# Kernel tuning notes

Hardware: AMD Instinct MI355X
Metric: run time of the kernel (lower is better)

## Reference

```python
import jax, jax.numpy as jnp
import numpy as np

N, E, D_IN, D_POS, LATENT, C = 50000, 800000, 500, 2, 128, 10
NEG_SLOPE = 0.2

def _glorot(key, shape):
    lim = np.sqrt(6.0 / (shape[0] + shape[1]))
    return jax.random.uniform(key, shape, jnp.float32, -lim, lim)

def setup_inputs() -> dict:
    key = jax.random.key(0)
    ks = jax.random.split(key, 20)
    x = jax.random.normal(ks[0], (N, D_IN), jnp.float32)
    pos = jax.random.uniform(ks[1], (N, D_POS), jnp.float32)
    edge_index = jax.random.randint(ks[2], (2, E), 0, N, jnp.int32)
    edge_attr = jax.random.uniform(ks[3], (E, 1), jnp.float32)
    d0 = D_IN + D_POS
    params = dict(
        W1=_glorot(ks[4], (d0, 512)), b1=jnp.zeros((512,)),
        W2=_glorot(ks[5], (512, 256)), b2=jnp.zeros((256,)),
        W3=_glorot(ks[6], (256, LATENT)), b3=jnp.zeros((LATENT,)),
        Wl=_glorot(ks[7], (LATENT, LATENT)), bl=jnp.zeros((LATENT,)),
        Wr=_glorot(ks[8], (LATENT, LATENT)), br=jnp.zeros((LATENT,)),
        We=_glorot(ks[9], (1, LATENT)),
        att=_glorot(ks[10], (LATENT, 1))[:, 0],
        bg=jnp.zeros((LATENT,)),
        Wd1=_glorot(ks[11], (LATENT, 64)), bd1=jnp.zeros((64,)),
        Wd2=_glorot(ks[12], (64, C)), bd2=jnp.zeros((C,)),
    )
    return dict(x=x, pos=pos, edge_index=edge_index, edge_attr=edge_attr, **params)

def _gatv2(h, src, dst, edge_attr, Wl, bl, Wr, br, We, att, bg):
    n = h.shape[0]
    xl = h @ Wl + bl            # [N, D] source transform
    xr = h @ Wr + br            # [N, D] target transform
    e = edge_attr @ We          # [E, D] edge embedding
    m = xl[src] + xr[dst] + e   # [E, D]
    m = jnp.where(m > 0, m, NEG_SLOPE * m)   # leaky_relu
    s = m @ att                 # [E] attention logits
    smax = jax.lax.stop_gradient(jax.ops.segment_max(s, dst, num_segments=n))
    ex = jnp.exp(s - smax[dst])
    denom = jax.ops.segment_sum(ex, dst, num_segments=n)
    alpha = ex / denom[dst]     # edge softmax over incoming edges
    out = jax.ops.segment_sum(alpha[:, None] * xl[src], dst, num_segments=n)
    return out + bg

def reference(x, pos, edge_index, edge_attr,
              W1, b1, W2, b2, W3, b3,
              Wl, bl, Wr, br, We, att, bg,
              Wd1, bd1, Wd2, bd2):
    xin = jnp.concatenate([x, pos], axis=-1)
    # encoder MLP [-1,512,256,latent], plain_last=True
    h = jax.nn.relu(xin @ W1 + b1)
    h = jax.nn.relu(h @ W2 + b2)
    h = h @ W3 + b3
    # GATv2 spatial channel, then block activation (plain_last=False)
    src, dst = edge_index[0], edge_index[1]
    h = _gatv2(h, src, dst, edge_attr, Wl, bl, Wr, br, We, att, bg)
    z = jax.nn.relu(h)
    # decoder MLP latent->64->C, plain_last, then softmax
    d = jax.nn.relu(z @ Wd1 + bd1)
    logits = d @ Wd2 + bd2
    return jax.nn.softmax(logits, axis=-1)
```

## Files before the change

### kernel.cpp

```cpp
#include <hip/hip_runtime.h>
#include <hip/hip_bf16.h>

#define NEG_SLOPE 0.2f

typedef _Float16 half8   __attribute__((ext_vector_type(8)));
typedef _Float16 half2v  __attribute__((ext_vector_type(2)));
typedef float    float4v __attribute__((ext_vector_type(4)));

__device__ __forceinline__ void gload16(const _Float16* g, _Float16* l)
{
    __builtin_amdgcn_global_load_lds(
        (const __attribute__((address_space(1))) unsigned int*)g,
        (__attribute__((address_space(3))) unsigned int*)l, 16, 0, 0);
}

__global__ __launch_bounds__(256)
void concat_f16_kernel(const float* __restrict__ x, const float* __restrict__ pos,
                       _Float16* __restrict__ A0, int N)
{
    const int total = N * 256;
    for (int i = blockIdx.x * 256 + threadIdx.x; i < total; i += gridDim.x * 256) {
        int node = i >> 8;
        int c2   = (i & 255) * 2;
        float2 v = make_float2(0.f, 0.f);
        if (c2 < 500)       v = *(const float2*)(x + (size_t)node * 500 + c2);
        else if (c2 == 500) v = *(const float2*)(pos + (size_t)node * 2);
        half2v h; h.x = (_Float16)v.x; h.y = (_Float16)v.y;
        *(half2v*)(A0 + (size_t)node * 512 + c2) = h;
    }
}

__global__ void wconv_kernel(const float* __restrict__ W, _Float16* __restrict__ Wt,
                             int K, int Nout, int Kpad)
{
    int total = Nout * Kpad;
    for (int i = blockIdx.x * blockDim.x + threadIdx.x; i < total;
         i += gridDim.x * blockDim.x) {
        int n = i / Kpad, k = i - n * Kpad;
        Wt[i] = (_Float16)((k < K) ? W[(size_t)k * Nout + n] : 0.f);
    }
}

__global__ __launch_bounds__(256)
void wfold_kernel(const float* __restrict__ W3, const float* __restrict__ Wl,
                  const float* __restrict__ Wr, _Float16* __restrict__ Wct)
{
    __shared__ float colv[128];
    const int nn = blockIdx.x;
    const float* Ws = (nn < 128) ? Wl : Wr;
    const int c = nn & 127;
    if (threadIdx.x < 128) colv[threadIdx.x] = Ws[threadIdx.x * 128 + c];
    __syncthreads();
    const int k2 = threadIdx.x;
    const float* wrow = W3 + k2 * 128;
    float s = 0.f;
    #pragma unroll 8
    for (int j = 0; j < 128; ++j) s += wrow[j] * colv[j];
    Wct[nn * 256 + k2] = (_Float16)s;
}

__global__ void bfold_kernel(const float* __restrict__ Wl, const float* __restrict__ Wr,
                             const float* __restrict__ b3, const float* __restrict__ bl,
                             const float* __restrict__ br, float* __restrict__ bcombo)
{
    int nn = threadIdx.x;
    const float* Ws = (nn < 128) ? Wl : Wr;
    int c = nn & 127;
    float s = (nn < 128) ? bl[c] : br[c];
    for (int j = 0; j < 128; ++j) s += b3[j] * Ws[j * 128 + c];
    bcombo[nn] = s;
}

__device__ inline void decode_swz(int b, int nblk, int ny, int& bx, int& by)
{
    int q = nblk >> 3, r = nblk & 7;
    int xcd = b & 7, j = b >> 3;
    int L = (xcd < r ? xcd * (q + 1) : r * (q + 1) + (xcd - r) * q) + j;
    bx = L / ny;
    by = L - bx * ny;
}

template<int WF32, int WF16>
__global__ __launch_bounds__(256)
void gemm_f16_kernel(const _Float16* __restrict__ A, const _Float16* __restrict__ Bt,
                     const float* __restrict__ bias, float* __restrict__ Cf,
                     _Float16* __restrict__ Ch, int M, int N, int K, int ny, int do_relu)
{
    __shared__ __align__(16) _Float16 smem[3][8192];

    int bx, by;
    decode_swz(blockIdx.x, gridDim.x, ny, bx, by);

    const int t    = threadIdx.x;
    const int row0 = bx * 128;
    const int n0   = by * 128;
    const int lane = t & 63;
    const int w    = t >> 6;
    const int wrow = (w >> 1) * 64;
    const int wcol = (w & 1) * 64;
    const int lrow = lane & 15;
    const int lk   = lane >> 4;
    const int sw   = lk ^ ((lrow >> 1) & 3);

    const int rl     = lane >> 2;
    const int lk_log = (lane & 3) ^ ((lane >> 3) & 3);

    int rA0 = row0 + w * 16 + rl;        if (rA0 > M - 1) rA0 = M - 1;
    int rA1 = row0 + (w + 4) * 16 + rl;  if (rA1 > M - 1) rA1 = M - 1;
    int rB0 = n0 + w * 16 + rl;          if (rB0 > N - 1) rB0 = N - 1;
    int rB1 = n0 + (w + 4) * 16 + rl;    if (rB1 > N - 1) rB1 = N - 1;

    const _Float16* gA0 = A  + (size_t)rA0 * K + lk_log * 8;
    const _Float16* gA1 = A  + (size_t)rA1 * K + lk_log * 8;
    const _Float16* gB0 = Bt + (size_t)rB0 * K + lk_log * 8;
    const _Float16* gB1 = Bt + (size_t)rB1 * K + lk_log * 8;

    float4v acc[4][4];
    #pragma unroll
    for (int i = 0; i < 4; ++i)
        #pragma unroll
        for (int j = 0; j < 4; ++j)
            acc[i][j] = (float4v){0.f, 0.f, 0.f, 0.f};

    const int KT = K >> 5;

    auto stage = [&](int kt, int buf) {
        _Float16* sA = &smem[buf][0];
        _Float16* sB = &smem[buf][4096];
        int ko = kt * 32;
        gload16(gA0 + ko, sA + (w    ) * 512);
        gload16(gA1 + ko, sA + (w + 4) * 512);
        gload16(gB0 + ko, sB + (w    ) * 512);
        gload16(gB1 + ko, sB + (w + 4) * 512);
    };

    stage(0, 0);
    if (KT > 1) {
        stage(1, 1);
        asm volatile("s_waitcnt vmcnt(4)" ::: "memory");
    } else {
        asm volatile("s_waitcnt vmcnt(0)" ::: "memory");
    }
    __builtin_amdgcn_sched_barrier(0);
    __builtin_amdgcn_s_barrier();

    for (int kt = 0; kt < KT; ++kt) {
        if (kt + 2 < KT) stage(kt + 2, (kt + 2) % 3);

        const _Float16* bufA = &smem[kt % 3][0];
        const _Float16* bufB = &smem[kt % 3][4096];

        half8 af[4], bf[4];
        #pragma unroll
        for (int mi = 0; mi < 4; ++mi)
            af[mi] = *(const half8*)(bufA + (wrow + mi * 16 + lrow) * 32 + sw * 8);
        #pragma unroll
        for (int ni = 0; ni < 4; ++ni)
            bf[ni] = *(const half8*)(bufB + (wcol + ni * 16 + lrow) * 32 + sw * 8);

        #pragma unroll
        for (int mi = 0; mi < 4; ++mi)
            #pragma unroll
            for (int ni = 0; ni < 4; ++ni)
                acc[mi][ni] = __builtin_amdgcn_mfma_f32_16x16x32_f16(
                    af[mi], bf[ni], acc[mi][ni], 0, 0, 0);

        if (kt + 1 < KT) {
            if (kt + 2 < KT) asm volatile("s_waitcnt vmcnt(4)" ::: "memory");
            else             asm volatile("s_waitcnt vmcnt(0)" ::: "memory");
            __builtin_amdgcn_sched_barrier(0);
            __builtin_amdgcn_s_barrier();
        }
    }

    #pragma unroll
    for (int mi = 0; mi < 4; ++mi) {
        #pragma unroll
        for (int ni = 0; ni < 4; ++ni) {
            #pragma unroll
            for (int r = 0; r < 4; ++r) {
                int row = row0 + wrow + mi * 16 + lk * 4 + r;
                int col = n0 + wcol + ni * 16 + lrow;
                if (row < M && col < N) {
                    float v = acc[mi][ni][r] + bias[col];
                    if (do_relu) v = fmaxf(v, 0.f);
                    if (WF32) Cf[(size_t)row * N + col] = v;
                    if (WF16) Ch[(size_t)row * N + col] = (_Float16)v;
                }
            }
        }
    }
}

__global__ __launch_bounds__(256)
void dec_fused_kernel(const _Float16* __restrict__ zh, const _Float16* __restrict__ Wd1t,
                      const float* __restrict__ bd1, const float* __restrict__ Wd2,
                      const float* __restrict__ bd2, float* __restrict__ out, int n)
{
    __shared__ __align__(16) _Float16 zs[128 * 40];
    __shared__ __align__(16) _Float16 wd1s[64 * 136];
    __shared__ __align__(16) _Float16 dsd[128 * 66];
    __shared__ float wd2s[640];
    __shared__ float bd1s[64];
    __shared__ float bd2s[10];

    const int t    = threadIdx.x;
    const int lane = t & 63;
    const int w    = t >> 6;
    const int wrow = (w >> 1) * 64;
    const int wcol = (w & 1) * 32;
    const int lrow = lane & 15;
    const int lk   = lane >> 4;
    const int node0 = blockIdx.x * 128;

    for (int i = t; i < 64 * 16; i += 256) {
        int r = i >> 4, c8 = i & 15;
        *(half8*)&wd1s[r * 136 + c8 * 8] = *(const half8*)(Wd1t + r * 128 + c8 * 8);
    }
    for (int i = t; i < 640; i += 256) wd2s[i] = Wd2[i];
    if (t < 64) bd1s[t] = bd1[t];
    if (t < 10) bd2s[t] = bd2[t];

    float4v acc[4][2];
    #pragma unroll
    for (int i = 0; i < 4; ++i)
        #pragma unroll
        for (int j = 0; j < 2; ++j)
            acc[i][j] = (float4v){0.f, 0.f, 0.f, 0.f};

    const int zrow = t >> 1;
    const int ch   = t & 1;
    int gz = node0 + zrow; if (gz > n - 1) gz = n - 1;
    const _Float16* zsrc = zh + (size_t)gz * 128 + ch * 16;

    for (int kt = 0; kt < 4; ++kt) {
        __syncthreads();
        *(half8*)&zs[zrow * 40 + ch * 16]     = *(const half8*)(zsrc + kt * 32);
        *(half8*)&zs[zrow * 40 + ch * 16 + 8] = *(const half8*)(zsrc + kt * 32 + 8);
        __syncthreads();

        half8 af[4], bf[2];
        #pragma unroll
        for (int mi = 0; mi < 4; ++mi)
            af[mi] = *(const half8*)&zs[(wrow + mi * 16 + lrow) * 40 + lk * 8];
        #pragma unroll
        for (int ni = 0; ni < 2; ++ni)
            bf[ni] = *(const half8*)&wd1s[(wcol + ni * 16 + lrow) * 136 + kt * 32 + lk * 8];

        #pragma unroll
        for (int mi = 0; mi < 4; ++mi)
            #pragma unroll
            for (int ni = 0; ni < 2; ++ni)
                acc[mi][ni] = __builtin_amdgcn_mfma_f32_16x16x32_f16(
                    af[mi], bf[ni], acc[mi][ni], 0, 0, 0);
    }

    #pragma unroll
    for (int mi = 0; mi < 4; ++mi) {
        #pragma unroll
        for (int ni = 0; ni < 2; ++ni) {
            #pragma unroll
            for (int r = 0; r < 4; ++r) {
                int rr = wrow + mi * 16 + lk * 4 + r;
                int cc = wcol + ni * 16 + lrow;
                float v = fmaxf(acc[mi][ni][r] + bd1s[cc], 0.f);
                dsd[rr * 66 + cc] = (_Float16)v;
            }
        }
    }
    __syncthreads();

    if (t < 128) {
        int node = node0 + t;
        if (node < n) {
            float lg[10];
            #pragma unroll
            for (int c = 0; c < 10; ++c) lg[c] = bd2s[c];
            #pragma unroll
            for (int k8 = 0; k8 < 8; ++k8) {
                half8 dv = *(const half8*)&dsd[t * 66 + k8 * 8];
                #pragma unroll
                for (int j = 0; j < 8; ++j) {
                    float dj = (float)dv[j];
                    #pragma unroll
                    for (int c = 0; c < 10; ++c)
                        lg[c] += dj * wd2s[(k8 * 8 + j) * 10 + c];
                }
            }
            float mx = lg[0];
            #pragma unroll
            for (int c = 1; c < 10; ++c) mx = fmaxf(mx, lg[c]);
            float ssum = 0.f;
            #pragma unroll
            for (int c = 0; c < 10; ++c) { lg[c] = expf(lg[c] - mx); ssum += lg[c]; }
            float inv = 1.f / ssum;
            #pragma unroll
            for (int c = 0; c < 10; ++c)
                out[(size_t)node * 10 + c] = lg[c] * inv;
        }
    }
}

__global__ void init_cnt_kernel(int* cnt, int n)
{
    for (int i = blockIdx.x * blockDim.x + threadIdx.x; i < n;
         i += gridDim.x * blockDim.x)
        cnt[i] = 0;
}

__global__ void count_edges_kernel(const int* __restrict__ dst, int* cnt, int E)
{
    int e = blockIdx.x * blockDim.x + threadIdx.x;
    if (e < E) atomicAdd(&cnt[dst[e]], 1);
}

__global__ __launch_bounds__(256)
void block_sum_kernel(const int* __restrict__ cnt, int* __restrict__ bsum, int n)
{
    __shared__ int sh[256];
    int t = threadIdx.x;
    int i = blockIdx.x * 256 + t;
    sh[t] = (i < n) ? cnt[i] : 0;
    __syncthreads();
    #pragma unroll
    for (int off = 128; off > 0; off >>= 1) {
        if (t < off) sh[t] += sh[t + off];
        __syncthreads();
    }
    if (t == 0) bsum[blockIdx.x] = sh[0];
}

__global__ __launch_bounds__(256)
void scan_bsum_kernel(int* __restrict__ bsum, int* __restrict__ row_start, int nb, int n)
{
    __shared__ int sh[256];
    int t = threadIdx.x;
    int v = (t < nb) ? bsum[t] : 0;
    sh[t] = v;
    __syncthreads();
    #pragma unroll
    for (int off = 1; off < 256; off <<= 1) {
        int xv = (t >= off) ? sh[t - off] : 0;
        __syncthreads();
        sh[t] += xv;
        __syncthreads();
    }
    if (t < nb) bsum[t] = sh[t] - v;
    if (t == 255) row_start[n] = sh[255];
}

__global__ __launch_bounds__(256)
void scan_final_kernel(const int* __restrict__ cnt, const int* __restrict__ boff,
                       int* __restrict__ row_start, int* __restrict__ cursor, int n)
{
    __shared__ int sh[256];
    int t = threadIdx.x;
    int i = blockIdx.x * 256 + t;
    int v = (i < n) ? cnt[i] : 0;
    sh[t] = v;
    __syncthreads();
    #pragma unroll
    for (int off = 1; off < 256; off <<= 1) {
        int xv = (t >= off) ? sh[t - off] : 0;
        __syncthreads();
        sh[t] += xv;
        __syncthreads();
    }
    if (i < n) {
        int ex = boff[blockIdx.x] + sh[t] - v;
        row_start[i] = ex;
        cursor[i]    = ex;
    }
}

__global__ void scatter_edges_kernel(const int* __restrict__ dst, const int* __restrict__ src,
                                     const float* __restrict__ ea, int* cursor,
                                     int2* __restrict__ recs, int E)
{
    int e = blockIdx.x * blockDim.x + threadIdx.x;
    if (e < E) {
        int p = atomicAdd(&cursor[dst[e]], 1);
        recs[p] = make_int2(src[e], __float_as_int(ea[e]));
    }
}

__global__ __launch_bounds__(256)
void gat_aggregate_kernel(const _Float16* __restrict__ xlr, const int2* __restrict__ recs,
                          const float* __restrict__ We, const float* __restrict__ att,
                          const float* __restrict__ bg, const int* __restrict__ row_start,
                          _Float16* __restrict__ z, int n)
{
    const int wave = threadIdx.x >> 6;
    const int lane = threadIdx.x & 63;
    const int node = blockIdx.x * 4 + wave;
    if (node >= n) return;

    const int g  = lane >> 4;
    const int sl = lane & 15;
    const int d0 = sl * 8;

    half2v at_h[4], we_h[4], xr_h[4];
    {
        float4 a0 = *(const float4*)(att + d0);
        float4 a1 = *(const float4*)(att + d0 + 4);
        float4 w0 = *(const float4*)(We + d0);
        float4 w1 = *(const float4*)(We + d0 + 4);
        at_h[0] = (half2v){(_Float16)a0.x, (_Float16)a0.y};
        at_h[1] = (half2v){(_Float16)a0.z, (_Float16)a0.w};
        at_h[2] = (half2v){(_Float16)a1.x, (_Float16)a1.y};
        at_h[3] = (half2v){(_Float16)a1.z, (_Float16)a1.w};
        we_h[0] = (half2v){(_Float16)w0.x, (_Float16)w0.y};
        we_h[1] = (half2v){(_Float16)w0.z, (_Float16)w0.w};
        we_h[2] = (half2v){(_Float16)w1.x, (_Float16)w1.y};
        we_h[3] = (half2v){(_Float16)w1.z, (_Float16)w1.w};
        half8 xh = *(const half8*)(xlr + (size_t)node * 256 + 128 + d0);
        #pragma unroll
        for (int q = 0; q < 4; ++q)
            xr_h[q] = (half2v){xh[2 * q], xh[2 * q + 1]};
    }
    const half2v slope2 = (half2v){(_Float16)NEG_SLOPE, (_Float16)NEG_SLOPE};

    const int beg = row_start[node];
    const int end = row_start[node + 1];

    float m_run = -INFINITY;
    float l_run = 0.f;
    float acc[8];
    #pragma unroll
    for (int j = 0; j < 8; ++j) acc[j] = 0.f;

    for (int idx = beg + g; idx < end; idx += 4) {
        int2 rec = recs[idx];
        _Float16 eh = (_Float16)__int_as_float(rec.y);
        half2v e2 = (half2v){eh, eh};
        half8 xh = *(const half8*)(xlr + (size_t)rec.x * 256 + d0);

        float part = 0.f;
        #pragma unroll
        for (int q = 0; q < 4; ++q) {
            half2v xq = (half2v){xh[2 * q], xh[2 * q + 1]};
            half2v mq = xq + (e2 * we_h[q] + xr_h[q]);
            half2v lq = __builtin_elementwise_max(mq, mq * slope2);
#if __has_builtin(__builtin_amdgcn_fdot2)
            part = __builtin_amdgcn_fdot2(lq, at_h[q], part, false);
#else
            part += (float)lq.x * (float)at_h[q].x + (float)lq.y * (float)at_h[q].y;
#endif
        }
        part += __shfl_xor(part, 1);
        part += __shfl_xor(part, 2);
        part += __shfl_xor(part, 4);
        part += __shfl_xor(part, 8);

        if (part <= m_run + 8.f) {
            float p = __expf(part - m_run);
            l_run += p;
            #pragma unroll
            for (int j = 0; j < 8; ++j) acc[j] += p * (float)xh[j];
        } else {
            float sc = __expf(m_run - part);
            l_run = l_run * sc + 1.f;
            #pragma unroll
            for (int j = 0; j < 8; ++j) acc[j] = acc[j] * sc + (float)xh[j];
            m_run = part;
        }
    }

    #pragma unroll
    for (int off = 16; off <= 32; off <<= 1) {
        float m_o = __shfl_xor(m_run, off);
        float l_o = __shfl_xor(l_run, off);
        float mn  = fmaxf(m_run, m_o);
        float sa  = (m_run == mn) ? 1.f : __expf(m_run - mn);
        float sb  = (m_o   == mn) ? 1.f : __expf(m_o - mn);
        l_run = l_run * sa + l_o * sb;
        #pragma unroll
        for (int j = 0; j < 8; ++j) {
            float a_o = __shfl_xor(acc[j], off);
            acc[j] = acc[j] * sa + a_o * sb;
        }
        m_run = mn;
    }

    if (g == 0) {
        float inv = (l_run > 0.f) ? 1.f / l_run : 0.f;
        const float* bgp = bg + d0;
        half8 o;
        #pragma unroll
        for (int j = 0; j < 8; ++j) {
            float v = fmaxf(acc[j] * inv + bgp[j], 0.f);
            o[j] = (_Float16)v;
        }
        *(half8*)(z + (size_t)node * 128 + d0) = o;
    }
}

extern "C" void kernel_launch(void* const* d_in, const int* in_sizes, int n_in,
                              void* d_out, int out_size, void* d_ws, size_t ws_size,
                              hipStream_t stream)
{
    const float* x    = (const float*)d_in[0];
    const float* pos  = (const float*)d_in[1];
    const int*   ei   = (const int*)d_in[2];
    const float* ea   = (const float*)d_in[3];
    const float* W1   = (const float*)d_in[4];
    const float* b1   = (const float*)d_in[5];
    const float* W2   = (const float*)d_in[6];
    const float* b2   = (const float*)d_in[7];
    const float* W3   = (const float*)d_in[8];
    const float* b3   = (const float*)d_in[9];
    const float* Wl   = (const float*)d_in[10];
    const float* bl   = (const float*)d_in[11];
    const float* Wr   = (const float*)d_in[12];
    const float* br   = (const float*)d_in[13];
    const float* We   = (const float*)d_in[14];
    const float* att  = (const float*)d_in[15];
    const float* bg   = (const float*)d_in[16];
    const float* Wd1  = (const float*)d_in[17];
    const float* bd1  = (const float*)d_in[18];
    const float* Wd2  = (const float*)d_in[19];
    const float* bd2  = (const float*)d_in[20];
    float* out = (float*)d_out;

    const int N = in_sizes[0] / 500;
    const int E = in_sizes[2] / 2;

    char* base = (char*)d_ws;
    const size_t szR = (size_t)N * 512 * 2;
    _Float16* A0h = (_Float16*)(base);
    _Float16* h2h = (_Float16*)(base);
    _Float16* zh  = (_Float16*)(base + (size_t)N * 384 * 2);
    char* r1 = base + szR;
    _Float16* h1h = (_Float16*)(r1);
    _Float16* xlr = (_Float16*)(r1);
    char* r2 = base + 2 * szR;
    _Float16* W1t   = (_Float16*)(r2);
    _Float16* W2t   = W1t  + 512 * 512;
    _Float16* Wct   = W2t  + 256 * 512;
    _Float16* Wd1t  = Wct  + 256 * 256;
    float*    bcombo = (float*)(Wd1t + 64 * 128);
    int* cnt       = (int*)(r2 + 2 * 1024 * 1024);
    int* row_start = cnt + N;
    int* bsum      = row_start + N + 1;
    int2* recs     = (int2*)(r2 + 3 * 1024 * 1024);

    const int* srcArr = ei;
    const int* dstArr = ei + E;
    const int gx = (N + 127) / 128;
    const int nb = (N + 255) / 256;

    concat_f16_kernel<<<2048, 256, 0, stream>>>(x, pos, A0h, N);
    wconv_kernel<<<1024, 256, 0, stream>>>(W1,  W1t,  502, 512, 512);
    wconv_kernel<<<512,  256, 0, stream>>>(W2,  W2t,  512, 256, 512);
    wconv_kernel<<<32,   256, 0, stream>>>(Wd1, Wd1t, 128, 64,  128);
    wfold_kernel<<<256, 256, 0, stream>>>(W3, Wl, Wr, Wct);
    bfold_kernel<<<1, 256, 0, stream>>>(Wl, Wr, b3, bl, br, bcombo);

    init_cnt_kernel<<<256, 256, 0, stream>>>(cnt, N);
    count_edges_kernel<<<(E + 255) / 256, 256, 0, stream>>>(dstArr, cnt, E);
    block_sum_kernel<<<nb, 256, 0, stream>>>(cnt, bsum, N);
    scan_bsum_kernel<<<1, 256, 0, stream>>>(bsum, row_start, nb, N);
    scan_final_kernel<<<nb, 256, 0, stream>>>(cnt, bsum, row_start, cnt, N);
    scatter_edges_kernel<<<(E + 255) / 256, 256, 0, stream>>>(dstArr, srcArr, ea, cnt, recs, E);

    gemm_f16_kernel<0,1><<<gx * 4, 256, 0, stream>>>(A0h, W1t, b1, nullptr, h1h, N, 512, 512, 4, 1);
    gemm_f16_kernel<0,1><<<gx * 2, 256, 0, stream>>>(h1h, W2t, b2, nullptr, h2h, N, 256, 512, 2, 1);
    gemm_f16_kernel<0,1><<<gx * 2, 256, 0, stream>>>(h2h, Wct, bcombo, nullptr, xlr, N, 256, 256, 2, 0);

    gat_aggregate_kernel<<<(N + 3) / 4, 256, 0, stream>>>(xlr, recs, We, att, bg,
                                                          row_start, zh, N);

    dec_fused_kernel<<<gx, 256, 0, stream>>>(zh, Wd1t, bd1, Wd2, bd2, out, N);
}
```

Before: 333.1 us.

## Fuse input concat and fp16 conversion into first encoder GEMM

Removes the separate concat kernel that converted x and pos to a padded fp16 buffer. A dedicated GEMM kernel now reads fp32 x and pos directly, converts them to fp16 in registers and stages them through LDS. This drops one full write and read of the fp16 activation matrix. In exchange, each column tile block re-reads the wider fp32 input, and the new kernel uses a simpler register-staged, single-buffered pipeline with two barriers per k-step instead of the tuned template GEMM.

```diff
diff --git a/kernel.cpp b/kernel.cpp
--- a/kernel.cpp
+++ b/kernel.cpp
@@ -12,22 +12,6 @@
     __builtin_amdgcn_global_load_lds(
         (const __attribute__((address_space(1))) unsigned int*)g,
         (__attribute__((address_space(3))) unsigned int*)l, 16, 0, 0);
-}
-
-__global__ __launch_bounds__(256)
-void concat_f16_kernel(const float* __restrict__ x, const float* __restrict__ pos,
-                       _Float16* __restrict__ A0, int N)
-{
-    const int total = N * 256;
-    for (int i = blockIdx.x * 256 + threadIdx.x; i < total; i += gridDim.x * 256) {
-        int node = i >> 8;
-        int c2   = (i & 255) * 2;
-        float2 v = make_float2(0.f, 0.f);
-        if (c2 < 500)       v = *(const float2*)(x + (size_t)node * 500 + c2);
-        else if (c2 == 500) v = *(const float2*)(pos + (size_t)node * 2);
-        half2v h; h.x = (_Float16)v.x; h.y = (_Float16)v.y;
-        *(half2v*)(A0 + (size_t)node * 512 + c2) = h;
-    }
 }
 
 __global__ void wconv_kernel(const float* __restrict__ W, _Float16* __restrict__ Wt,
@@ -78,6 +62,128 @@
     int L = (xcd < r ? xcd * (q + 1) : r * (q + 1) + (xcd - r) * q) + j;
     bx = L / ny;
     by = L - bx * ny;
+}
+
+__global__ __launch_bounds__(256)
+void gemm1_concat_kernel(const float* __restrict__ xf, const float* __restrict__ posf,
+                         const _Float16* __restrict__ Bt, const float* __restrict__ bias,
+                         _Float16* __restrict__ Ch, int M, int ny)
+{
+    const int K = 512, N = 512;
+    __shared__ __align__(16) _Float16 As[128 * 40];
+    __shared__ __align__(16) _Float16 Bs[128 * 40];
+
+    int bx, by;
+    decode_swz(blockIdx.x, gridDim.x, ny, bx, by);
+
+    const int t    = threadIdx.x;
+    const int row0 = bx * 128;
+    const int n0   = by * 128;
+    const int lane = t & 63;
+    const int w    = t >> 6;
+    const int wrow = (w >> 1) * 64;
+    const int wcol = (w & 1) * 64;
+    const int lrow = lane & 15;
+    const int lk   = lane >> 4;
+
+    const int r0 = t >> 2;
+    const int kq = t & 3;
+
+    float4v acc[4][4];
+    #pragma unroll
+    for (int i = 0; i < 4; ++i)
+        #pragma unroll
+        for (int j = 0; j < 4; ++j)
+            acc[i][j] = (float4v){0.f, 0.f, 0.f, 0.f};
+
+    const int KT = 16;
+    half8 ra[2], rb[2];
+
+    int grA[2], grB[2];
+    #pragma unroll
+    for (int i = 0; i < 2; ++i) {
+        int gr = row0 + r0 + i * 64; if (gr > M - 1) gr = M - 1;
+        grA[i] = gr;
+        grB[i] = n0 + r0 + i * 64;
+    }
+
+    auto load_tile = [&](int kt) {
+        int kb = kt * 32 + kq * 8;
+        #pragma unroll
+        for (int i = 0; i < 2; ++i) {
+            half8 ha;
+            if (kb + 7 < 500) {
+                const float* src = xf + (size_t)grA[i] * 500 + kb;
+                float4 a = *(const float4*)src;
+                float4 b = *(const float4*)(src + 4);
+                ha[0] = (_Float16)a.x; ha[1] = (_Float16)a.y;
+                ha[2] = (_Float16)a.z; ha[3] = (_Float16)a.w;
+                ha[4] = (_Float16)b.x; ha[5] = (_Float16)b.y;
+                ha[6] = (_Float16)b.z; ha[7] = (_Float16)b.w;
+            } else {
+                #pragma unroll
+                for (int j = 0; j < 8; ++j) {
+                    int k = kb + j;
+                    float v = 0.f;
+                    if (k < 500)      v = xf[(size_t)grA[i] * 500 + k];
+                    else if (k < 502) v = posf[(size_t)grA[i] * 2 + (k - 500)];
+                    ha[j] = (_Float16)v;
+                }
+            }
+            ra[i] = ha;
+            rb[i] = *(const half8*)(Bt + (size_t)grB[i] * K + kb);
+        }
+    };
+    auto store_tile = [&]() {
+        #pragma unroll
+        for (int i = 0; i < 2; ++i) {
+            int row = r0 + i * 64;
+            *(half8*)&As[row * 40 + kq * 8] = ra[i];
+            *(half8*)&Bs[row * 40 + kq * 8] = rb[i];
+        }
+    };
+
+    load_tile(0);
+    store_tile();
+    __syncthreads();
+
+    for (int kt = 0; kt < KT; ++kt) {
+        if (kt + 1 < KT) load_tile(kt + 1);
+
+        half8 af[4], bf[4];
+        #pragma unroll
+        for (int mi = 0; mi < 4; ++mi)
+            af[mi] = *(const half8*)&As[(wrow + mi * 16 + lrow) * 40 + lk * 8];
+        #pragma unroll
+        for (int ni = 0; ni < 4; ++ni)
+            bf[ni] = *(const half8*)&Bs[(wcol + ni * 16 + lrow) * 40 + lk * 8];
+
+        #pragma unroll
+        for (int mi = 0; mi < 4; ++mi)
+            #pragma unroll
+            for (int ni = 0; ni < 4; ++ni)
+                acc[mi][ni] = __builtin_amdgcn_mfma_f32_16x16x32_f16(
+                    af[mi], bf[ni], acc[mi][ni], 0, 0, 0);
+
+        __syncthreads();
+        if (kt + 1 < KT) { store_tile(); __syncthreads(); }
+    }
+
+    #pragma unroll
+    for (int mi = 0; mi < 4; ++mi) {
+        #pragma unroll
+        for (int ni = 0; ni < 4; ++ni) {
+            #pragma unroll
+            for (int r = 0; r < 4; ++r) {
+                int row = row0 + wrow + mi * 16 + lk * 4 + r;
+                int col = n0 + wcol + ni * 16 + lrow;
+                if (row < M) {
+                    float v = fmaxf(acc[mi][ni][r] + bias[col], 0.f);
+                    Ch[(size_t)row * N + col] = (_Float16)v;
+                }
+            }
+        }
+    }
 }
 
 template<int WF32, int WF16>
@@ -527,7 +633,6 @@
 
     char* base = (char*)d_ws;
     const size_t szR = (size_t)N * 512 * 2;
-    _Float16* A0h = (_Float16*)(base);
     _Float16* h2h = (_Float16*)(base);
     _Float16* zh  = (_Float16*)(base + (size_t)N * 384 * 2);
     char* r1 = base + szR;
@@ -549,7 +654,6 @@
     const int gx = (N + 127) / 128;
     const int nb = (N + 255) / 256;
 
-    concat_f16_kernel<<<2048, 256, 0, stream>>>(x, pos, A0h, N);
     wconv_kernel<<<1024, 256, 0, stream>>>(W1,  W1t,  502, 512, 512);
     wconv_kernel<<<512,  256, 0, stream>>>(W2,  W2t,  512, 256, 512);
     wconv_kernel<<<32,   256, 0, stream>>>(Wd1, Wd1t, 128, 64,  128);
@@ -563,7 +667,7 @@
     scan_final_kernel<<<nb, 256, 0, stream>>>(cnt, bsum, row_start, cnt, N);
     scatter_edges_kernel<<<(E + 255) / 256, 256, 0, stream>>>(dstArr, srcArr, ea, cnt, recs, E);
 
-    gemm_f16_kernel<0,1><<<gx * 4, 256, 0, stream>>>(A0h, W1t, b1, nullptr, h1h, N, 512, 512, 4, 1);
+    gemm1_concat_kernel<<<gx * 4, 256, 0, stream>>>(x, pos, W1t, b1, h1h, N, 4);
     gemm_f16_kernel<0,1><<<gx * 2, 256, 0, stream>>>(h1h, W2t, b2, nullptr, h2h, N, 256, 512, 2, 1);
     gemm_f16_kernel<0,1><<<gx * 2, 256, 0, stream>>>(h2h, Wct, bcombo, nullptr, xlr, N, 256, 256, 2, 0);
 
```

After: 342.5 us. 1.03x slower.
